# Optimization experiments

Measured on AMD Instinct MI355X. Metric: run time of the kernel, lower is better.

Reference implementation:

```python
import jax, jax.numpy as jnp
import numpy as np

B, L, D, H = 1, 1024, 768, 12
h = D // H  # 64
EPS = 1e-5
ALPHA = 0.01  # leaky relu slope


def setup_inputs() -> dict:
    key = jax.random.key(0)
    ks = jax.random.split(key, 10)
    s = 0.02
    f32 = jnp.float32
    return {
        "x": jax.random.normal(ks[0], (B, L, D), f32),
        "filters": jax.random.normal(ks[1], (L, h), f32) * s,  # spectral filters [L, h]
        "wq_w": jax.random.normal(ks[2], (D, D), f32) * s,
        "wq_b": jnp.zeros((D,), f32),
        "wk_w": jax.random.normal(ks[3], (D, D), f32) * s,
        "wk_b": jnp.zeros((D,), f32),
        "wv_w": jax.random.normal(ks[4], (D, D), f32) * s,
        "wv_b": jnp.zeros((D,), f32),
        "wo_w": jax.random.normal(ks[5], (D, D), f32) * s,
        "wo_b": jnp.zeros((D,), f32),
        "wg_w": jax.random.normal(ks[6], (h * h, 1), f32) * s,
        "wg_b": jnp.zeros((1,), f32),
        "qk_scale": jnp.ones((1, H, 1), f32) + jax.random.normal(ks[7], (1, H, 1), f32) * 0.02,
        "kv_scale": jnp.ones((1, H, 1, 1, 1), f32) + jax.random.normal(ks[8], (1, H, 1, 1, 1), f32) * 0.02,
    }


def _causal_fft_conv(f, u):
    """Per-head-channel causal FFT convolution. f: [L,h], u: [B,H,L,h] -> [B,H,L,h]."""
    n = 2 * L  # >= L + L - 1 for linear (full) convolution
    Ff = jnp.fft.rfft(f, n=n, axis=0)            # [n//2+1, h]
    Uf = jnp.fft.rfft(u, n=n, axis=2)            # [B,H,n//2+1,h]
    y = jnp.fft.irfft(Uf * Ff[None, None], n=n, axis=2)
    return y[:, :, :L, :]


def _l2norm(t):
    # matches F.normalize(dim=-1): x / max(||x||, 1e-12)
    nrm = jnp.sqrt(jnp.sum(t * t, axis=-1, keepdims=True))
    return t / jnp.maximum(nrm, 1e-12)


def _combine(a, b):
    """Associative combine: (m, s, n, Z, g) running-max / exp-sum / exp-weighted-v / outer-product / gate-sum."""
    m_x, s_x, n_x, Z_x, g_x = a
    m_y, s_y, n_y, Z_y, g_y = b
    m = jnp.maximum(m_x, m_y)
    ex = jnp.exp(m_x - m)
    ey = jnp.exp(m_y - m)
    return (m,
            s_x * ex + s_y * ey,
            n_x * ex[..., None] + n_y * ey[..., None],
            Z_x + Z_y,
            g_x + g_y)


def reference(x, filters, wq_w, wq_b, wk_w, wk_b, wv_w, wv_b, wo_w, wo_b,
              wg_w, wg_b, qk_scale, kv_scale):
    # split heads: [B,H,L,h]
    bhld = x.reshape(B, L, H, h).transpose(0, 2, 1, 3)
    # spectral filtering (tensordot_conv): per-channel causal conv with filters
    xt = _causal_fft_conv(filters, bhld)                       # [B,H,L,h]
    xt = xt.transpose(0, 2, 1, 3).reshape(B, L, D)             # [B,L,D]

    q = (xt @ wq_w + wq_b).reshape(B, L, H, h).transpose(0, 2, 1, 3)
    k = (xt @ wk_w + wk_b).reshape(B, L, H, h).transpose(0, 2, 1, 3)
    v = (xt @ wv_w + wv_b).reshape(B, L, H, h).transpose(0, 2, 1, 3)
    q, k, v = _l2norm(q), _l2norm(k), _l2norm(v)

    sim = jnp.einsum('bhld,bhld->bhl', q, k) * qk_scale         # [B,H,L]
    # Z[b,h,s,p,n] = v[b,h,s,p] * k[b,h,s,n]
    Z = jnp.einsum('bhsn,bhsp->bhspn', k, v) * kv_scale         # [B,H,L,h,h]

    gate_logits = Z.reshape(B, H, L, h * h) @ wg_w + wg_b       # [B,H,L,1]
    gl = jnp.where(gate_logits > 0, gate_logits, ALPHA * gate_logits)
    gates = (gl * gl + EPS)[..., 0]                             # [B,H,L]
    gated_Z = Z * gates[..., None, None]

    leaves = (sim, jnp.ones_like(sim), v, gated_Z, gates)
    m_s, s_s, n_s, Z_s, g_s = jax.lax.associative_scan(_combine, leaves, axis=2)

    linear_attn = n_s / (s_s[..., None] + EPS)                  # [B,H,L,h]
    softmax_w = jnp.exp(sim - m_s) / (s_s + EPS)                # [B,H,L]
    Hm = Z_s / (g_s[..., None, None] + EPS)                     # [B,H,L,h,h]
    ctx = jnp.einsum('bhtp,bhtpn->bhtn', q, Hm)                 # [B,H,L,h]
    qla = linear_attn
    lerp = ctx + (qla - ctx) * softmax_w[..., None]

    y = lerp.transpose(0, 2, 1, 3).reshape(B, L, D)
    return y @ wo_w + wo_b
```

## Files before the change

### kernel.cpp

```cpp
#include <hip/hip_runtime.h>
#include <hip/hip_bf16.h>

constexpr int LS = 1024;
constexpr int DM = 768;
constexpr int NH = 12;
constexpr int HD = 64;
constexpr float EPSF = 1e-5f;
constexpr float ALPHAF = 0.01f;

constexpr int SG = 16;
constexpr int NTL = LS / SG;
constexpr int WSZ = DM * DM;
constexpr int NPAR = 8;

typedef unsigned short u16;
typedef __attribute__((ext_vector_type(8))) short bf16x8;
typedef __attribute__((ext_vector_type(8))) unsigned short u16x8;
typedef __attribute__((ext_vector_type(4))) float f32x4;

__device__ __forceinline__ u16 f2b(float f) {
  unsigned u = __float_as_uint(f);
  u += 0x7FFFu + ((u >> 16) & 1u);
  return (u16)(u >> 16);
}
__device__ __forceinline__ float b2f(u16 b) {
  return __uint_as_float((unsigned)b << 16);
}

__device__ __forceinline__ void gld16(const u16* g, void* l) {
  __builtin_amdgcn_global_load_lds(
      (const __attribute__((address_space(1))) void*)g,
      (__attribute__((address_space(3))) void*)l, 16, 0, 0);
}

__global__ __launch_bounds__(256) void conv_txw_kernel(
    const float* __restrict__ x, const float* __restrict__ f,
    const float* __restrict__ wq, const float* __restrict__ wk,
    const float* __restrict__ wv, const float* __restrict__ wo,
    u16* __restrict__ wT, u16* __restrict__ pbase) {
  extern __shared__ char smem[];
  const int b = blockIdx.x;
  const int tid = threadIdx.x;

  if (b >= 1536) {
    const int b2 = b - 1536;
    const int kb = (b2 % 12) * 64, nb = ((b2 / 12) % 12) * 64, z = b2 / 144;
    const float* src = (z == 0) ? wq : (z == 1) ? wk : (z == 2) ? wv : wo;
    u16* dst = wT + (size_t)z * WSZ;
    float (*T)[65] = (float(*)[65])smem;
#pragma unroll
    for (int rep = 0; rep < 4; ++rep) {
      const int r = rep * 16 + (tid >> 4);
      const int c4 = (tid & 15) * 4;
      const float4 v4 = *(const float4*)(src + (size_t)(kb + r) * DM + nb + c4);
      T[r][c4] = v4.x; T[r][c4 + 1] = v4.y; T[r][c4 + 2] = v4.z; T[r][c4 + 3] = v4.w;
    }
    __syncthreads();
#pragma unroll
    for (int rep = 0; rep < 4; ++rep) {
      const int n = rep * 16 + (tid >> 4);
      const int k4 = (tid & 15) * 4;
      ushort4 o;
      o.x = f2b(T[k4 + 0][n]); o.y = f2b(T[k4 + 1][n]);
      o.z = f2b(T[k4 + 2][n]); o.w = f2b(T[k4 + 3][n]);
      *(ushort4*)(dst + (size_t)(nb + n) * DM + kb + k4) = o;
    }
    return;
  }

  const int i    = b & 15;
  const int head = (b >> 4) % 12;
  const int par  = b / 192;
  const int c    = tid & 63;
  const int sg   = tid >> 6;
  const int tbase = i * 64;
  const int l0w   = tbase + sg * 16;
  u16* __restrict__ xt_p = pbase + (size_t)par * LS * DM;

  float4 (*Xs2)[64] = (float4(*)[64])smem;

  {
    const float4 z4 = make_float4(0.f, 0.f, 0.f, 0.f);
#pragma unroll
    for (int k = 0; k < 3; ++k) {
      const int lin = k * 256 + tid;
      const int g   = lin >> 6;
      const int cc  = lin & 63;
      const int grp = (g < 4) ? g : (16 + g);
      Xs2[grp][cc] = z4;
    }
  }

  float acc[16];
#pragma unroll
  for (int t = 0; t < 16; ++t) acc[t] = 0.f;

  const float* xg   = x + head * HD + c;
  const float* fcol = f + c;

  for (int j = par; j <= i; j += NPAR) {
    const int sbase = j * 64;
    const int b0 = (j < i) ? (tbase - sbase - 64) : 0;
#pragma unroll
    for (int k = 0; k < 4; ++k) {
      const int m  = sg + 4 * k;
      const int ss = 4 * m;
      float4 v4;
      v4.x = xg[(sbase + ss + 0) * DM];
      v4.y = xg[(sbase + ss + 1) * DM];
      v4.z = xg[(sbase + ss + 2) * DM];
      v4.w = xg[(sbase + ss + 3) * DM];
      Xs2[4 + m][c] = v4;
    }
    __syncthreads();

    const int dstart = (j < i) ? (b0 + sg * 16) : 0;
    const int nsteps = (j < i) ? 5 : (sg + 1);
    for (int k = 0; k < nsteps; ++k) {
      const int d0    = dstart + 16 * k;
      const int rbase = l0w - d0 - sbase;
      float fr[16];
#pragma unroll
      for (int m = 0; m < 16; ++m) fr[m] = fcol[(d0 + m) * HD];
      float xw[32];
      const int xgb = rbase >> 2;
#pragma unroll
      for (int m = 0; m < 8; ++m) {
        const float4 v4 = Xs2[xgb + m][c];
        xw[4 * m + 0] = v4.x; xw[4 * m + 1] = v4.y;
        xw[4 * m + 2] = v4.z; xw[4 * m + 3] = v4.w;
      }
#pragma unroll
      for (int li = 0; li < 16; ++li)
#pragma unroll
        for (int dd = 0; dd < 16; ++dd)
          acc[li] = fmaf(fr[dd], xw[li - dd + 16], acc[li]);
    }
    __syncthreads();
  }

#pragma unroll
  for (int li = 0; li < 16; ++li)
    xt_p[(size_t)(l0w + li) * DM + head * HD + c] = f2b(acc[li]);
}

__global__ __launch_bounds__(256) void pack_xt(const u16* __restrict__ pbase,
                                               u16* __restrict__ xtb) {
  const size_t NT = (size_t)LS * DM;
  const size_t i = ((size_t)blockIdx.x * 256 + threadIdx.x) * 8;
  float s[8] = {};
#pragma unroll
  for (int p = 0; p < NPAR; ++p) {
    const u16x8 v8 = *(const u16x8*)(pbase + p * NT + i);
#pragma unroll
    for (int e = 0; e < 8; ++e) s[e] += b2f(v8[e]);
  }
  u16x8 o;
#pragma unroll
  for (int e = 0; e < 8; ++e) o[e] = f2b(s[e]);
  *(u16x8*)(xtb + i) = o;
}

__global__ __launch_bounds__(256) void qkv_mfma(const u16* __restrict__ xtb,
                                                const u16* __restrict__ wT,
                                                const float* __restrict__ bq,
                                                const float* __restrict__ bk,
                                                const float* __restrict__ bv,
                                                float* __restrict__ qo,
                                                float* __restrict__ ko,
                                                float* __restrict__ vo) {
  const int b = blockIdx.x;
  const int xcd = b & 7, j = b >> 3;
  const int rt = (xcd & 3) * 4 + j / 6;
  const int ct = (xcd >> 2) * 6 + j % 6;

  __shared__ u16 As[64 * 64];
  __shared__ u16 Bs[3][64 * 64];

  const int tid = threadIdx.x, w = tid >> 6, l = tid & 63;
  const int wr = w >> 1, wc = w & 1;

  const int srow1 = tid >> 3, sc16 = tid & 7;
  const int c16L1 = sc16 ^ (srow1 & 7);
  const int srow2 = srow1 + 32;
  const int c16L2 = sc16 ^ (srow2 & 7);

  const u16* Ag1 = xtb + (size_t)(rt * 64 + srow1) * DM + c16L1 * 8;
  const u16* Ag2 = xtb + (size_t)(rt * 64 + srow2) * DM + c16L2 * 8;

  char* lA = (char*)As + w * 1024;

  f32x4 acc[3][2][2] = {};
  for (int kb = 0; kb < DM; kb += 64) {
    gld16(Ag1 + kb, lA);
    gld16(Ag2 + kb, lA + 4096);
#pragma unroll
    for (int z = 0; z < 3; ++z) {
      const u16* wz = wT + (size_t)z * WSZ;
      const u16* Bg1 = wz + (size_t)(ct * 64 + srow1) * DM + c16L1 * 8;
      const u16* Bg2 = wz + (size_t)(ct * 64 + srow2) * DM + c16L2 * 8;
      char* lB = (char*)Bs[z] + w * 1024;
      gld16(Bg1 + kb, lB);
      gld16(Bg2 + kb, lB + 4096);
    }
    __syncthreads();
#pragma unroll
    for (int kk = 0; kk < 2; ++kk) {
      bf16x8 a[2];
#pragma unroll
      for (int ar = 0; ar < 2; ++ar) {
        const int row = wr * 32 + ar * 16 + (l & 15);
        const int c16 = ((kk << 2) + (l >> 4)) ^ (row & 7);
        a[ar] = *(const bf16x8*)((char*)As + row * 128 + c16 * 16);
      }
#pragma unroll
      for (int z = 0; z < 3; ++z) {
        bf16x8 bb[2];
#pragma unroll
        for (int bc = 0; bc < 2; ++bc) {
          const int col = wc * 32 + bc * 16 + (l & 15);
          const int c16 = ((kk << 2) + (l >> 4)) ^ (col & 7);
          bb[bc] = *(const bf16x8*)((char*)Bs[z] + col * 128 + c16 * 16);
        }
#pragma unroll
        for (int ar = 0; ar < 2; ++ar)
#pragma unroll
          for (int bc = 0; bc < 2; ++bc)
            acc[z][ar][bc] = __builtin_amdgcn_mfma_f32_16x16x32_bf16(
                a[ar], bb[bc], acc[z][ar][bc], 0, 0, 0);
      }
    }
    __syncthreads();
  }

  const float* biasArr[3] = {bq, bk, bv};
  float* outArr[3] = {qo, ko, vo};
  const int rbase = rt * 64 + wr * 32 + ((l >> 4) << 2);
  const int cb = wc * 32 + (l & 15);
#pragma unroll
  for (int z = 0; z < 3; ++z) {
    const float* bias = biasArr[z];
    float* out = outArr[z];
#pragma unroll
    for (int ar = 0; ar < 2; ++ar)
#pragma unroll
      for (int bc = 0; bc < 2; ++bc) {
        const int col = cb + bc * 16;
        const float bbv = bias[ct * 64 + col];
#pragma unroll
        for (int r = 0; r < 4; ++r)
          out[((size_t)ct * LS + rbase + ar * 16 + r) * HD + col] =
              acc[z][ar][bc][r] + bbv;
      }
  }
}

__global__ __launch_bounds__(256) void out_mfma(const u16* __restrict__ lerpb,
                                                const u16* __restrict__ woT,
                                                const float* __restrict__ bias,
                                                float* __restrict__ out) {
  const int b = blockIdx.x;
  const int xcd = b & 7, j = b >> 3;
  const int unit = xcd * 3 + (j >> 3), sub = j & 7;
  const int ct = unit >> 1, rt = (unit & 1) * 8 + sub;

  __shared__ u16 As[64 * 64];
  __shared__ u16 Bs[64 * 64];

  const int tid = threadIdx.x, w = tid >> 6, l = tid & 63;
  const int wr = w >> 1, wc = w & 1;

  const int srow1 = tid >> 3, sc16 = tid & 7;
  const int c16L1 = sc16 ^ (srow1 & 7);
  const int srow2 = srow1 + 32;
  const int c16L2 = sc16 ^ (srow2 & 7);

  const u16* Ag1 = lerpb + (size_t)(rt * 64 + srow1) * DM + c16L1 * 8;
  const u16* Ag2 = lerpb + (size_t)(rt * 64 + srow2) * DM + c16L2 * 8;
  const u16* Bg1 = woT + (size_t)(ct * 64 + srow1) * DM + c16L1 * 8;
  const u16* Bg2 = woT + (size_t)(ct * 64 + srow2) * DM + c16L2 * 8;

  char* lA = (char*)As + w * 1024;
  char* lB = (char*)Bs + w * 1024;

  f32x4 acc[2][2] = {};
  for (int kb = 0; kb < DM; kb += 64) {
    gld16(Ag1 + kb, lA);
    gld16(Ag2 + kb, lA + 4096);
    gld16(Bg1 + kb, lB);
    gld16(Bg2 + kb, lB + 4096);
    __syncthreads();
#pragma unroll
    for (int kk = 0; kk < 2; ++kk) {
      bf16x8 a[2], bb[2];
#pragma unroll
      for (int ar = 0; ar < 2; ++ar) {
        const int row = wr * 32 + ar * 16 + (l & 15);
        const int c16 = ((kk << 2) + (l >> 4)) ^ (row & 7);
        a[ar] = *(const bf16x8*)((char*)As + row * 128 + c16 * 16);
      }
#pragma unroll
      for (int bc = 0; bc < 2; ++bc) {
        const int col = wc * 32 + bc * 16 + (l & 15);
        const int c16 = ((kk << 2) + (l >> 4)) ^ (col & 7);
        bb[bc] = *(const bf16x8*)((char*)Bs + col * 128 + c16 * 16);
      }
#pragma unroll
      for (int ar = 0; ar < 2; ++ar)
#pragma unroll
        for (int bc = 0; bc < 2; ++bc)
          acc[ar][bc] = __builtin_amdgcn_mfma_f32_16x16x32_bf16(
              a[ar], bb[bc], acc[ar][bc], 0, 0, 0);
    }
    __syncthreads();
  }

  const int rbase = rt * 64 + wr * 32 + ((l >> 4) << 2);
  const int cb = wc * 32 + (l & 15);
#pragma unroll
  for (int ar = 0; ar < 2; ++ar)
#pragma unroll
    for (int bc = 0; bc < 2; ++bc) {
      const int col = ct * 64 + cb + bc * 16;
      const float bbv = bias[col];
#pragma unroll
      for (int r = 0; r < 4; ++r)
        out[(size_t)(rbase + ar * 16 + r) * DM + col] = acc[ar][bc][r] + bbv;
    }
}

__global__ __launch_bounds__(256) void nsg_state_kernel(
    float* __restrict__ q, float* __restrict__ k, float* __restrict__ v,
    const float* __restrict__ wg, const float* __restrict__ wgb,
    const float* __restrict__ qk_scale, const float* __restrict__ kv_scale,
    float* __restrict__ sim, float* __restrict__ gates,
    float* __restrict__ states, float* __restrict__ nes) {
  const int j = blockIdx.x, head = blockIdx.y;
  const int s0 = j * SG;
  const int tid = threadIdx.x;
  const int wid = tid >> 6, lane = tid & 63;
  __shared__ alignas(16) float Vs[SG][68];
  __shared__ alignas(16) float Kg[SG][68];
  __shared__ float Es[SG];

  auto red = [](float x) {
#pragma unroll
    for (int o = 32; o; o >>= 1) x += __shfl_xor(x, o);
    return x;
  };

  const float qks = qk_scale[head], kvs = kv_scale[head], wb = wgb[0];
#pragma unroll
  for (int it = 0; it < 4; ++it) {
    const int rr = wid * 4 + it;
    const size_t idx = ((size_t)head * LS + s0 + rr) * HD + lane;
    float qv = q[idx], kv = k[idx], vv = v[idx];
    const float qn = fmaxf(sqrtf(red(qv * qv)), 1e-12f);
    const float kn = fmaxf(sqrtf(red(kv * kv)), 1e-12f);
    const float vn = fmaxf(sqrtf(red(vv * vv)), 1e-12f);
    qv /= qn; kv /= kn; vv /= vn;
    q[idx] = qv; k[idx] = kv; v[idx] = vv;
    const float s = red(qv * kv) * qks;
    Vs[rr][lane] = vv;
    float t = 0.f;
#pragma unroll 8
    for (int p = 0; p < 64; ++p) t = fmaf(Vs[rr][p], wg[p * 64 + lane], t);
    float gl = red(t * kv) * kvs + wb;
    gl = gl > 0.f ? gl : ALPHAF * gl;
    const float g = gl * gl + EPSF;
    Kg[rr][lane] = kv * g;
    if (lane == 0) {
      sim[head * LS + s0 + rr] = s;
      gates[head * LS + s0 + rr] = g;
      Es[rr] = expf(s);
    }
  }
  __syncthreads();

  const int p0 = (tid >> 4) * 4, n0 = (tid & 15) * 4;
  float acc[4][4] = {};
  for (int s = 0; s < SG; ++s) {
    const float4 ra = *(const float4*)&Vs[s][p0];
    const float4 rb = *(const float4*)&Kg[s][n0];
    const float av[4] = {ra.x, ra.y, ra.z, ra.w};
    const float bv[4] = {rb.x, rb.y, rb.z, rb.w};
#pragma unroll
    for (int i = 0; i < 4; ++i)
#pragma unroll
      for (int jj = 0; jj < 4; ++jj)
        acc[i][jj] = fmaf(av[i], bv[jj], acc[i][jj]);
  }
  float* Sout = states + (size_t)(head * NTL + j) * 4096;
#pragma unroll
  for (int i = 0; i < 4; ++i)
    *(float4*)&Sout[(p0 + i) * 64 + n0] =
        make_float4(acc[i][0], acc[i][1], acc[i][2], acc[i][3]);

  if (tid < HD) {
    float ne = 0.f;
#pragma unroll
    for (int s = 0; s < SG; ++s) ne = fmaf(Es[s], Vs[s][tid], ne);
    nes[(size_t)(head * NTL + j) * HD + tid] = ne;
  }
}

__global__ __launch_bounds__(1024) void scan_prefix_kernel(
    const float* __restrict__ sim, const float* __restrict__ gates,
    float* __restrict__ m_s, float* __restrict__ Sraw, float* __restrict__ g_s,
    float* __restrict__ states, float* __restrict__ nes) {
  const int head = blockIdx.x, chunk = blockIdx.y;
  const int tid = threadIdx.x, lane = tid & 63, wid = tid >> 6;

  if (chunk == 0) {
    __shared__ float wm[16], wS[16], wg2[16];
    const float sv = sim[head * LS + tid];
    float m = sv, S = expf(sv), g = gates[head * LS + tid];
#pragma unroll
    for (int off = 1; off < 64; off <<= 1) {
      const float pm = __shfl_up(m, off);
      const float pS = __shfl_up(S, off);
      const float pg = __shfl_up(g, off);
      if (lane >= off) { m = fmaxf(m, pm); S += pS; g += pg; }
    }
    if (lane == 63) { wm[wid] = m; wS[wid] = S; wg2[wid] = g; }
    __syncthreads();
    for (int w2 = 0; w2 < wid; ++w2) {
      m = fmaxf(m, wm[w2]); S += wS[w2]; g += wg2[w2];
    }
    m_s[head * LS + tid] = m;
    Sraw[head * LS + tid] = S;
    g_s[head * LS + tid] = g;

    if (tid < HD) {
      float a = 0.f;
      float* nb = nes + (size_t)head * NTL * HD + tid;
#pragma unroll 4
      for (int jj = 0; jj < NTL; ++jj) {
        float* p = nb + (size_t)jj * HD;
        const float t = *p;
        *p = a;
        a += t;
      }
    }
  }

  {
    float a = 0.f;
    float* base = states + (size_t)head * NTL * 4096 + chunk * 1024 + tid;
#pragma unroll 4
    for (int jj = 0; jj < NTL; ++jj) {
      float* p = base + (size_t)jj * 4096;
      const float t = *p;
      *p = a;
      a += t;
    }
  }
}

__global__ __launch_bounds__(256) void apply_kernel(const float* __restrict__ q,
                                                    const float* __restrict__ k,
                                                    const float* __restrict__ v,
                                                    const float* __restrict__ sim,
                                                    const float* __restrict__ gates,
                                                    const float* __restrict__ m_s,
                                                    const float* __restrict__ Sraw,
                                                    const float* __restrict__ g_s,
                                                    const float* __restrict__ states,
                                                    const float* __restrict__ nes,
                                                    const float* __restrict__ kv_scale,
                                                    u16* __restrict__ lerpb) {
  const int bt = blockIdx.x, head = blockIdx.y;
  const int t0 = bt * SG;
  const int tid = threadIdx.x;
  __shared__ alignas(16) float Ps[64][68];
  __shared__ alignas(16) float Qs[SG][68];
  __shared__ alignas(16) float Vs[SG][68];
  __shared__ alignas(16) float Ks[SG][68];
  __shared__ alignas(16) float NEp[64];
  __shared__ float Ag[SG][SG + 1];
  __shared__ float Es[SG], Gs[SG];

  const float* Pg = states + (size_t)(head * NTL + bt) * 4096;
#pragma unroll
  for (int rep = 0; rep < 4; ++rep) {
    const int lin = rep * 1024 + tid * 4;
    *(float4*)&Ps[lin >> 6][lin & 63] = *(const float4*)(Pg + lin);
  }
  {
    const int r = tid >> 4, c = (tid & 15) * 4;
    const size_t rowbase = ((size_t)head * LS + t0 + r) * HD;
    *(float4*)&Qs[r][c] = *(const float4*)(q + rowbase + c);
    *(float4*)&Ks[r][c] = *(const float4*)(k + rowbase + c);
    *(float4*)&Vs[r][c] = *(const float4*)(v + rowbase + c);
  }
  if (tid < SG) {
    Es[tid] = expf(sim[head * LS + t0 + tid]);
    Gs[tid] = gates[head * LS + t0 + tid];
  }
  if (tid < HD) NEp[tid] = nes[(size_t)(head * NTL + bt) * HD + tid];
  __syncthreads();

  {
    const int t = tid >> 4, s = tid & 15;
    float a = 0.f;
    if (s <= t) {
#pragma unroll
      for (int p = 0; p < 64; p += 4) {
        const float4 q4 = *(const float4*)&Qs[t][p];
        const float4 v4 = *(const float4*)&Vs[s][p];
        a = fmaf(q4.x, v4.x, a); a = fmaf(q4.y, v4.y, a);
        a = fmaf(q4.z, v4.z, a); a = fmaf(q4.w, v4.w, a);
      }
      a *= Gs[s];
    }
    Ag[t][s] = a;
  }
  __syncthreads();

  const int r = tid >> 4, c0 = (tid & 15) * 4;
  float4 O = make_float4(0.f, 0.f, 0.f, 0.f);
#pragma unroll 8
  for (int p = 0; p < 64; ++p) {
    const float qv = Qs[r][p];
    const float4 p4 = *(const float4*)&Ps[p][c0];
    O.x = fmaf(qv, p4.x, O.x); O.y = fmaf(qv, p4.y, O.y);
    O.z = fmaf(qv, p4.z, O.z); O.w = fmaf(qv, p4.w, O.w);
  }
  float4 Nn = *(const float4*)&NEp[c0];
  for (int s = 0; s <= r; ++s) {
    const float ag = Ag[r][s];
    const float es = Es[s];
    const float4 k4 = *(const float4*)&Ks[s][c0];
    const float4 v4 = *(const float4*)&Vs[s][c0];
    O.x = fmaf(ag, k4.x, O.x); O.y = fmaf(ag, k4.y, O.y);
    O.z = fmaf(ag, k4.z, O.z); O.w = fmaf(ag, k4.w, O.w);
    Nn.x = fmaf(es, v4.x, Nn.x); Nn.y = fmaf(es, v4.y, Nn.y);
    Nn.z = fmaf(es, v4.z, Nn.z); Nn.w = fmaf(es, v4.w, Nn.w);
  }

  const int t = t0 + r;
  const float m  = m_s[head * LS + t];
  const float em = expf(-m);
  const float ss = Sraw[head * LS + t] * em;
  const float inv = 1.f / (ss + EPSF);
  const float sw  = expf(sim[head * LS + t] - m) * inv;
  const float gi  = kv_scale[head] / (g_s[head * LS + t] + EPSF);
  const float ei  = em * inv;
  float rx, ry, rz, rw;
  { const float cx = O.x * gi, la = Nn.x * ei; rx = cx + (la - cx) * sw; }
  { const float cx = O.y * gi, la = Nn.y * ei; ry = cx + (la - cx) * sw; }
  { const float cx = O.z * gi, la = Nn.z * ei; rz = cx + (la - cx) * sw; }
  { const float cx = O.w * gi, la = Nn.w * ei; rw = cx + (la - cx) * sw; }
  ushort4 ob;
  ob.x = f2b(rx); ob.y = f2b(ry); ob.z = f2b(rz); ob.w = f2b(rw);
  *(ushort4*)&lerpb[(size_t)t * DM + head * HD + c0] = ob;
}

extern "C" void kernel_launch(void* const* d_in, const int* in_sizes, int n_in,
                              void* d_out, int out_size, void* d_ws, size_t ws_size,
                              hipStream_t stream) {
  (void)in_sizes; (void)n_in; (void)out_size; (void)ws_size;
  const float* x        = (const float*)d_in[0];
  const float* filters  = (const float*)d_in[1];
  const float* wq_w     = (const float*)d_in[2];
  const float* wq_b     = (const float*)d_in[3];
  const float* wk_w     = (const float*)d_in[4];
  const float* wk_b     = (const float*)d_in[5];
  const float* wv_w     = (const float*)d_in[6];
  const float* wv_b     = (const float*)d_in[7];
  const float* wo_w     = (const float*)d_in[8];
  const float* wo_b     = (const float*)d_in[9];
  const float* wg_w     = (const float*)d_in[10];
  const float* wg_b     = (const float*)d_in[11];
  const float* qk_scale = (const float*)d_in[12];
  const float* kv_scale = (const float*)d_in[13];

  float* ws = (float*)d_ws;
  const size_t NT = (size_t)LS * DM;
  float* q     = ws;
  float* k     = ws + NT;
  float* v     = ws + 2 * NT;
  float* sim   = ws + 3 * NT;
  float* gates = sim + NH * LS;
  float* m_s   = gates + NH * LS;
  float* Sraw  = m_s + NH * LS;
  float* g_s   = Sraw + NH * LS;
  float* states = g_s + NH * LS;
  float* nes    = states + (size_t)NH * NTL * 4096;
  u16*   xtb    = (u16*)(nes + (size_t)NH * NTL * HD);
  u16*   wT     = xtb + NT;
  u16*   lerpb  = wT + 4 * (size_t)WSZ;
  u16*   pbase  = lerpb + NT;

  conv_txw_kernel<<<dim3(2112), 256, 28672, stream>>>(
      x, filters, wq_w, wk_w, wv_w, wo_w, wT, pbase);
  pack_xt<<<dim3(NT / 2048), 256, 0, stream>>>(pbase, xtb);
  qkv_mfma<<<dim3(192), 256, 0, stream>>>(xtb, wT, wq_b, wk_b, wv_b, q, k, v);
  nsg_state_kernel<<<dim3(NTL, NH), 256, 0, stream>>>(
      q, k, v, wg_w, wg_b, qk_scale, kv_scale, sim, gates, states, nes);
  scan_prefix_kernel<<<dim3(NH, 4), 1024, 0, stream>>>(
      sim, gates, m_s, Sraw, g_s, states, nes);
  apply_kernel<<<dim3(NTL, NH), 256, 0, stream>>>(
      q, k, v, sim, gates, m_s, Sraw, g_s, states, nes, kv_scale, lerpb);
  out_mfma<<<dim3(192), 256, 0, stream>>>(
      lerpb, wT + 3 * (size_t)WSZ, wo_b, (float*)d_out);
}
```

Baseline: 101.5 us.

## Restructure causal conv to per-wave 16-row chunks with register-only operands

The causal convolution part of the fused conv/transpose kernel now gives each wave its own 16-row output chunk and walks 16-sample input chunks strided by the partition count. It loads x and a 31-tap filter window straight from global memory into registers instead of staging x through shared memory. This removes the shared-memory staging, the zero-fill and the block-wide barriers, and lowers the dynamic shared-memory request. The cost is more redundant global loads per wave and a different load balance across the causal triangle, where each wave's work now depends on its own row.

```diff
diff --git a/kernel.cpp b/kernel.cpp
--- a/kernel.cpp
+++ b/kernel.cpp
@@ -68,80 +68,47 @@
     return;
   }
 
-  const int i    = b & 15;
+  const int lcg  = b & 15;
   const int head = (b >> 4) % 12;
   const int par  = b / 192;
-  const int c    = tid & 63;
-  const int sg   = tid >> 6;
-  const int tbase = i * 64;
-  const int l0w   = tbase + sg * 16;
+  const int lane = tid & 63;
+  const int wid  = tid >> 6;
+  const int lc   = lcg * 4 + wid;
+  const int l0   = lc * 16;
+
+  const float* xg = x + head * HD + lane;
+  const float* fg = f + lane;
+
+  float acc[16];
+#pragma unroll
+  for (int t = 0; t < 16; ++t) acc[t] = 0.f;
+
+  for (int sc = par; sc <= lc; sc += NPAR) {
+    const int s0 = sc * 16;
+    const int d0 = l0 - s0 - 15;
+    float xw[16], fr[31];
+#pragma unroll
+    for (int m = 0; m < 16; ++m) xw[m] = xg[(s0 + m) * DM];
+    if (sc < lc) {
+#pragma unroll
+      for (int m = 0; m < 31; ++m) fr[m] = fg[(d0 + m) * HD];
+    } else {
+#pragma unroll
+      for (int m = 0; m < 15; ++m) fr[m] = 0.f;
+#pragma unroll
+      for (int m = 15; m < 31; ++m) fr[m] = fg[(d0 + m) * HD];
+    }
+#pragma unroll
+    for (int li = 0; li < 16; ++li)
+#pragma unroll
+      for (int si = 0; si < 16; ++si)
+        acc[li] = fmaf(fr[li - si + 15], xw[si], acc[li]);
+  }
+
   u16* __restrict__ xt_p = pbase + (size_t)par * LS * DM;
-
-  float4 (*Xs2)[64] = (float4(*)[64])smem;
-
-  {
-    const float4 z4 = make_float4(0.f, 0.f, 0.f, 0.f);
-#pragma unroll
-    for (int k = 0; k < 3; ++k) {
-      const int lin = k * 256 + tid;
-      const int g   = lin >> 6;
-      const int cc  = lin & 63;
-      const int grp = (g < 4) ? g : (16 + g);
-      Xs2[grp][cc] = z4;
-    }
-  }
-
-  float acc[16];
-#pragma unroll
-  for (int t = 0; t < 16; ++t) acc[t] = 0.f;
-
-  const float* xg   = x + head * HD + c;
-  const float* fcol = f + c;
-
-  for (int j = par; j <= i; j += NPAR) {
-    const int sbase = j * 64;
-    const int b0 = (j < i) ? (tbase - sbase - 64) : 0;
-#pragma unroll
-    for (int k = 0; k < 4; ++k) {
-      const int m  = sg + 4 * k;
-      const int ss = 4 * m;
-      float4 v4;
-      v4.x = xg[(sbase + ss + 0) * DM];
-      v4.y = xg[(sbase + ss + 1) * DM];
-      v4.z = xg[(sbase + ss + 2) * DM];
-      v4.w = xg[(sbase + ss + 3) * DM];
-      Xs2[4 + m][c] = v4;
-    }
-    __syncthreads();
-
-    const int dstart = (j < i) ? (b0 + sg * 16) : 0;
-    const int nsteps = (j < i) ? 5 : (sg + 1);
-    for (int k = 0; k < nsteps; ++k) {
-      const int d0    = dstart + 16 * k;
-      const int rbase = l0w - d0 - sbase;
-      float fr[16];
-#pragma unroll
-      for (int m = 0; m < 16; ++m) fr[m] = fcol[(d0 + m) * HD];
-      float xw[32];
-      const int xgb = rbase >> 2;
-#pragma unroll
-      for (int m = 0; m < 8; ++m) {
-        const float4 v4 = Xs2[xgb + m][c];
-        xw[4 * m + 0] = v4.x; xw[4 * m + 1] = v4.y;
-        xw[4 * m + 2] = v4.z; xw[4 * m + 3] = v4.w;
-      }
-#pragma unroll
-      for (int li = 0; li < 16; ++li)
-#pragma unroll
-        for (int dd = 0; dd < 16; ++dd)
-          acc[li] = fmaf(fr[dd], xw[li - dd + 16], acc[li]);
-    }
-    __syncthreads();
-  }
-
 #pragma unroll
   for (int li = 0; li < 16; ++li)
-    xt_p[(size_t)(l0w + li) * DM + head * HD + c] = f2b(acc[li]);
+    xt_p[(size_t)(l0 + li) * DM + head * HD + lane] = f2b(acc[li]);
 }
 
 __global__ __launch_bounds__(256) void pack_xt(const u16* __restrict__ pbase,
@@ -592,7 +559,7 @@
   u16*   lerpb  = wT + 4 * (size_t)WSZ;
   u16*   pbase  = lerpb + NT;
 
-  conv_txw_kernel<<<dim3(2112), 256, 28672, stream>>>(
+  conv_txw_kernel<<<dim3(2112), 256, 16640, stream>>>(
       x, filters, wq_w, wk_w, wv_w, wo_w, wT, pbase);
   pack_xt<<<dim3(NT / 2048), 256, 0, stream>>>(pbase, xtb);
   qkv_mfma<<<dim3(192), 256, 0, stream>>>(xtb, wT, wq_b, wk_b, wv_b, q, k, v);
```

Result: no change. 103.1 us (+1.6%).
